# Kernel optimization log

Hardware: AMD Instinct MI355X
Metric: run time of the kernel (lower is better)

Reference implementation:

```python
import jax, jax.numpy as jnp
import numpy as np

N_NODES = 50000
N_EDGES = 800000
D_IN = 128
D_OUT = 128
BN_EPS = 1e-5


def setup_inputs() -> dict:
    key = jax.random.key(0)
    ks = jax.random.split(key, 8)
    node_feats = jax.random.normal(ks[0], (N_NODES, D_IN), dtype=jnp.float32)
    src = jax.random.randint(ks[1], (N_EDGES,), 0, N_NODES, dtype=jnp.int32)
    dst = jax.random.randint(ks[2], (N_EDGES,), 0, N_NODES, dtype=jnp.int32)
    # Glorot-ish init for weights
    scale = 1.0 / np.sqrt(D_IN)
    W = jax.random.normal(ks[3], (D_IN, D_OUT), dtype=jnp.float32) * scale
    b = jnp.zeros((D_OUT,), dtype=jnp.float32)
    Wr = jax.random.normal(ks[4], (D_IN, D_OUT), dtype=jnp.float32) * scale
    br = jnp.zeros((D_OUT,), dtype=jnp.float32)
    gamma = jnp.ones((D_OUT,), dtype=jnp.float32)
    beta = jnp.zeros((D_OUT,), dtype=jnp.float32)
    return {"node_feats": node_feats, "src": src, "dst": dst, "W": W, "b": b,
            "Wr": Wr, "br": br, "gamma": gamma, "beta": beta}


def reference(node_feats, src, dst, W, b, Wr, br, gamma, beta):
    N = node_feats.shape[0]
    ones_e = jnp.ones(src.shape[0], dtype=node_feats.dtype)
    # DGL GraphConv norm='both': D_out^{-1/2} on source side, D_in^{-1/2} on dest side
    deg_out = jnp.clip(jax.ops.segment_sum(ones_e, src, num_segments=N), 1.0)
    deg_in = jnp.clip(jax.ops.segment_sum(ones_e, dst, num_segments=N), 1.0)
    h = node_feats * jax.lax.rsqrt(deg_out)[:, None]        # [N, D_in]
    agg = jax.ops.segment_sum(h[src], dst, num_segments=N)  # gather + scatter-add, [N, D_in]
    agg = agg * jax.lax.rsqrt(deg_in)[:, None]
    gcn = jax.nn.relu(agg @ W + b)                           # GraphConv activation=relu
    res = jax.nn.relu(node_feats @ Wr + br)                  # residual branch
    y = gcn + res
    # BatchNorm1d (training mode: biased batch stats)
    mean = jnp.mean(y, axis=0)
    var = jnp.mean(jnp.square(y - mean), axis=0)
    out = (y - mean) * jax.lax.rsqrt(var + BN_EPS) * gamma + beta
    return out
```

## Files before the change

kernel.cpp:

```cpp
#include <hip/hip_runtime.h>

#define N_NODES 50000
#define N_EDGES 800000
#define D 128
#define BN_EPS 1e-5f
#define AGG_BLOCKS 2048
#define SCAN_BLOCKS 196
#define CHUNKS 64
#define EPC (N_EDGES / CHUNKS)
#define HALF_BINS 25600
#define HALF_U32 12800

typedef short bf16x8 __attribute__((ext_vector_type(8)));
typedef float f32x4  __attribute__((ext_vector_type(4)));


__global__ __launch_bounds__(256) void hist_kernel(
        const int* __restrict__ keys, unsigned int* __restrict__ hist) {
    __shared__ unsigned int h[HALF_U32];
    int tid = threadIdx.x;
    int c = blockIdx.x, r = blockIdx.y;
    for (int j = tid; j < HALF_U32; j += 256) h[j] = 0u;
    __syncthreads();
    int base = c * EPC;
    int lo = r * HALF_BINS;
    for (int i = tid; i < EPC; i += 256) {
        int b = keys[base + i] - lo;
        if ((unsigned)b < (unsigned)HALF_BINS)
            atomicAdd(&h[b >> 1], 1u << ((b & 1) * 16));
    }
    __syncthreads();
    unsigned int* out = hist + ((size_t)(r * CHUNKS + c)) * HALF_U32;
    for (int j = tid; j < HALF_U32; j += 256) out[j] = h[j];
}

__global__ __launch_bounds__(256) void merge_kernel(
        unsigned int* __restrict__ histD, unsigned int* __restrict__ histS,
        int* __restrict__ cnt_in, int* __restrict__ cnt_out) {
    int q = blockIdx.x * 256 + threadIdx.x;
    int r = blockIdx.y;
    unsigned int* hist = blockIdx.z ? histS : histD;
    int* cnt = blockIdx.z ? cnt_out : cnt_in;
    unsigned int lo = 0, hi = 0;
    for (int c = 0; c < CHUNKS; c++) {
        size_t idx = ((size_t)(r * CHUNKS + c)) * HALF_U32 + q;
        unsigned int v = hist[idx];
        hist[idx] = lo | (hi << 16);
        lo += v & 0xffffu; hi += v >> 16;
    }
    int n0 = r * HALF_BINS + q * 2;
    cnt[n0]     = (int)lo;
    cnt[n0 + 1] = (int)hi;
}

__global__ __launch_bounds__(256) void scan1_kernel(
        const int* __restrict__ cnt_in, int* __restrict__ row_ptr, int* __restrict__ blk_sum) {
    __shared__ int sh[256];
    int t = threadIdx.x;
    int i = blockIdx.x * 256 + t;
    int v = cnt_in[i];
    sh[t] = v;
    __syncthreads();
    int inc = v;
    #pragma unroll
    for (int off = 1; off < 256; off <<= 1) {
        int u = (t >= off) ? sh[t - off] : 0;
        __syncthreads();
        inc += u; sh[t] = inc;
        __syncthreads();
    }
    row_ptr[i] = inc - v;
    if (t == 255) blk_sum[blockIdx.x] = inc;
}

__global__ __launch_bounds__(256) void scan2_kernel(int* __restrict__ blk_sum, int* __restrict__ row_ptr) {
    __shared__ int sh[256];
    int t = threadIdx.x;
    int v = (t < SCAN_BLOCKS) ? blk_sum[t] : 0;
    sh[t] = v;
    __syncthreads();
    int inc = v;
    #pragma unroll
    for (int off = 1; off < 256; off <<= 1) {
        int u = (t >= off) ? sh[t - off] : 0;
        __syncthreads();
        inc += u; sh[t] = inc;
        __syncthreads();
    }
    if (t < SCAN_BLOCKS) blk_sum[t] = inc - v;
    if (t == 0) row_ptr[N_NODES] = N_EDGES;
}

__global__ __launch_bounds__(256) void scan3_kernel(
        const int* __restrict__ cnt_in, const int* __restrict__ cnt_out,
        const int* __restrict__ blk_sum, int* __restrict__ row_ptr,
        float* __restrict__ rin, float* __restrict__ rout) {
    int i = blockIdx.x * 256 + threadIdx.x;
    if (i < N_NODES) {
        row_ptr[i] = row_ptr[i] + blk_sum[blockIdx.x];
        int ci = cnt_in[i], co = cnt_out[i];
        rin[i]  = rsqrtf((float)(ci > 1 ? ci : 1));
        rout[i] = rsqrtf((float)(co > 1 ? co : 1));
    }
}

__global__ __launch_bounds__(512) void fill2_kernel(
        const int* __restrict__ src, const int* __restrict__ dst,
        const int* __restrict__ row_ptr, const unsigned int* __restrict__ histP,
        int* __restrict__ csr_src) {
    __shared__ unsigned int h[HALF_U32];
    int tid = threadIdx.x;
    int c = blockIdx.x;
    int base = c * EPC;
    for (int r = 0; r < 2; r++) {
        for (int j = tid; j < HALF_U32; j += 512) h[j] = 0u;
        __syncthreads();
        int lo = r * HALF_BINS;
        const unsigned int* pre_c = histP + ((size_t)(r * CHUNKS + c)) * HALF_U32;
        for (int i = tid; i < EPC; i += 512) {
            int d = dst[base + i];
            int b = d - lo;
            if ((unsigned)b < (unsigned)HALF_BINS) {
                int sh = (b & 1) * 16;
                unsigned int old = atomicAdd(&h[b >> 1], 1u << sh);
                unsigned int rank = (old >> sh) & 0xffffu;
                unsigned int pre = (pre_c[b >> 1] >> sh) & 0xffffu;
                int p = row_ptr[d] + (int)(pre + rank);
                csr_src[p] = src[base + i];
            }
        }
        __syncthreads();
    }
}

__device__ __forceinline__ unsigned int pack_rne(float a, float b) {
    unsigned int ua = __float_as_uint(a); ua += 0x7fffu + ((ua >> 16) & 1u);
    unsigned int ub = __float_as_uint(b); ub += 0x7fffu + ((ub >> 16) & 1u);
    return (ua >> 16) | (ub & 0xffff0000u);
}

__global__ __launch_bounds__(256) void pack_w(
        const float* __restrict__ W, const float* __restrict__ Wr,
        uint4* __restrict__ pW, uint4* __restrict__ pWr) {
    int t = blockIdx.x * 256 + threadIdx.x;
    const float* S = (t & 2048) ? Wr : W;
    uint4* Dst     = (t & 2048) ? pWr : pW;
    int e = t & 2047;
    int lane = e & 63, ks = (e >> 6) & 3, ct = e >> 8;
    int n  = ct * 16 + (lane & 15);
    int k0 = ks * 32 + (lane >> 4) * 8;
    float v[8];
    #pragma unroll
    for (int j = 0; j < 8; j++) v[j] = S[(k0 + j) * D + n];
    uint4 r;
    r.x = pack_rne(v[0], v[1]); r.y = pack_rne(v[2], v[3]);
    r.z = pack_rne(v[4], v[5]); r.w = pack_rne(v[6], v[7]);
    Dst[e] = r;
}

__global__ __launch_bounds__(256) void gemm_mfma(
        const float* __restrict__ x, const uint4* __restrict__ pW,
        const uint4* __restrict__ pWr, const float* __restrict__ br,
        const float* __restrict__ rout, unsigned short* __restrict__ hwb,
        float* __restrict__ res) {
    int tid = threadIdx.x, wid = tid >> 6, lane = tid & 63;
    int quad = lane >> 4, l15 = lane & 15;
    int r0 = blockIdx.x * 64 + wid * 16;
    int arow = r0 + l15; if (arow > N_NODES - 1) arow = N_NODES - 1;
    union { bf16x8 v; uint4 u; } A[4];
    const float* xrow = x + (size_t)arow * D;
    #pragma unroll
    for (int ks = 0; ks < 4; ks++) {
        float4 f0 = *(const float4*)(xrow + ks * 32 + quad * 8);
        float4 f1 = *(const float4*)(xrow + ks * 32 + quad * 8 + 4);
        A[ks].u.x = pack_rne(f0.x, f0.y); A[ks].u.y = pack_rne(f0.z, f0.w);
        A[ks].u.z = pack_rne(f1.x, f1.y); A[ks].u.w = pack_rne(f1.z, f1.w);
    }
    f32x4 accW[8], accR[8];
    #pragma unroll
    for (int ct = 0; ct < 8; ct++) { accW[ct] = (f32x4)0.f; accR[ct] = (f32x4)0.f; }
    #pragma unroll
    for (int ct = 0; ct < 8; ct++) {
        #pragma unroll
        for (int ks = 0; ks < 4; ks++) {
            union { bf16x8 v; uint4 u; } Bw, Br2;
            Bw.u  = pW [(ct * 4 + ks) * 64 + lane];
            Br2.u = pWr[(ct * 4 + ks) * 64 + lane];
            accW[ct] = __builtin_amdgcn_mfma_f32_16x16x32_bf16(A[ks].v, Bw.v,  accW[ct], 0, 0, 0);
            accR[ct] = __builtin_amdgcn_mfma_f32_16x16x32_bf16(A[ks].v, Br2.v, accR[ct], 0, 0, 0);
        }
    }
    float ro[4]; int rowok[4];
    #pragma unroll
    for (int reg = 0; reg < 4; reg++) {
        int row = r0 + quad * 4 + reg;
        rowok[reg] = row < N_NODES;
        ro[reg] = rout[rowok[reg] ? row : N_NODES - 1];
    }
    #pragma unroll
    for (int ct = 0; ct < 8; ct++) {
        int c = ct * 16 + l15;
        float brv = br[c];
        #pragma unroll
        for (int reg = 0; reg < 4; reg++) {
            int row = r0 + quad * 4 + reg;
            if (rowok[reg]) {
                float hv = accW[ct][reg] * ro[reg];
                unsigned int u = __float_as_uint(hv);
                u += 0x7fffu + ((u >> 16) & 1u);
                hwb[(size_t)row * D + c] = (unsigned short)(u >> 16);
                res[(size_t)row * D + c] = fmaxf(accR[ct][reg] + brv, 0.f);
            }
        }
    }
}

__device__ __forceinline__ float bf_lo(unsigned int v) { return __uint_as_float(v << 16); }
__device__ __forceinline__ float bf_hi(unsigned int v) { return __uint_as_float(v & 0xffff0000u); }

__device__ __forceinline__ void acc8(float* a, const uint4 v) {
    a[0] += bf_lo(v.x); a[1] += bf_hi(v.x);
    a[2] += bf_lo(v.y); a[3] += bf_hi(v.y);
    a[4] += bf_lo(v.z); a[5] += bf_hi(v.z);
    a[6] += bf_lo(v.w); a[7] += bf_hi(v.w);
}
__device__ __forceinline__ void acc8m(float* a, const uint4 v, float m) {
    a[0] = fmaf(m, bf_lo(v.x), a[0]); a[1] = fmaf(m, bf_hi(v.x), a[1]);
    a[2] = fmaf(m, bf_lo(v.y), a[2]); a[3] = fmaf(m, bf_hi(v.y), a[3]);
    a[4] = fmaf(m, bf_lo(v.z), a[4]); a[5] = fmaf(m, bf_hi(v.z), a[5]);
    a[6] = fmaf(m, bf_lo(v.w), a[6]); a[7] = fmaf(m, bf_hi(v.w), a[7]);
}

__device__ __forceinline__ int sel4(int qg, int i0, int i1, int i2, int i3) {
    int a = (qg & 1) ? i1 : i0;
    int b = (qg & 1) ? i3 : i2;
    return (qg & 2) ? b : a;
}

__global__ __launch_bounds__(256) void agg_kernel(
        const unsigned int* __restrict__ hwb, const int* __restrict__ row_ptr,
        const int* __restrict__ csr_src, const float* __restrict__ rin,
        const float* __restrict__ bias, float* __restrict__ y,
        float* __restrict__ parts) {
    __shared__ float red[4 * 256];
    int tid = threadIdx.x;
    int lane = tid & 63, wid = tid >> 6;
    int wave = blockIdx.x * 4 + wid;
    int nw = AGG_BLOCKS * 4;
    int qg = lane >> 4;
    int ql = lane & 15;
    float s1[8] = {0,0,0,0,0,0,0,0}, s2[8] = {0,0,0,0,0,0,0,0};
    float4 bv0, bv1;
    if (lane < 16) {
        bv0 = ((const float4*)bias)[2 * lane];
        bv1 = ((const float4*)bias)[2 * lane + 1];
    }
    for (int n = wave; n < N_NODES; n += nw) {
        int e0 = row_ptr[n], e1 = row_ptr[n + 1];
        float a[8] = {0,0,0,0,0,0,0,0};
        for (int j0 = e0; j0 < e1; j0 += 64) {
            int cnt = e1 - j0; if (cnt > 64) cnt = 64;
            int myidx = (lane < cnt) ? csr_src[j0 + lane] : 0;
            int i = 0;
            for (; i + 16 <= cnt; i += 16) {
                int p0 = sel4(qg, __builtin_amdgcn_readlane(myidx, i + 0),
                                  __builtin_amdgcn_readlane(myidx, i + 1),
                                  __builtin_amdgcn_readlane(myidx, i + 2),
                                  __builtin_amdgcn_readlane(myidx, i + 3));
                int p1 = sel4(qg, __builtin_amdgcn_readlane(myidx, i + 4),
                                  __builtin_amdgcn_readlane(myidx, i + 5),
                                  __builtin_amdgcn_readlane(myidx, i + 6),
                                  __builtin_amdgcn_readlane(myidx, i + 7));
                int p2 = sel4(qg, __builtin_amdgcn_readlane(myidx, i + 8),
                                  __builtin_amdgcn_readlane(myidx, i + 9),
                                  __builtin_amdgcn_readlane(myidx, i + 10),
                                  __builtin_amdgcn_readlane(myidx, i + 11));
                int p3 = sel4(qg, __builtin_amdgcn_readlane(myidx, i + 12),
                                  __builtin_amdgcn_readlane(myidx, i + 13),
                                  __builtin_amdgcn_readlane(myidx, i + 14),
                                  __builtin_amdgcn_readlane(myidx, i + 15));
                uint4 v0 = *((const uint4*)(hwb + (size_t)p0 * 64) + ql);
                uint4 v1 = *((const uint4*)(hwb + (size_t)p1 * 64) + ql);
                uint4 v2 = *((const uint4*)(hwb + (size_t)p2 * 64) + ql);
                uint4 v3 = *((const uint4*)(hwb + (size_t)p3 * 64) + ql);
                acc8(a, v0); acc8(a, v1); acc8(a, v2); acc8(a, v3);
            }
            for (; i + 4 <= cnt; i += 4) {
                int p0 = sel4(qg, __builtin_amdgcn_readlane(myidx, i + 0),
                                  __builtin_amdgcn_readlane(myidx, i + 1),
                                  __builtin_amdgcn_readlane(myidx, i + 2),
                                  __builtin_amdgcn_readlane(myidx, i + 3));
                uint4 v0 = *((const uint4*)(hwb + (size_t)p0 * 64) + ql);
                acc8(a, v0);
            }
            int t = cnt - i;
            if (t > 0) {
                int lim = cnt - 1;
                int j1 = i + 1 <= lim ? i + 1 : lim;
                int j2 = i + 2 <= lim ? i + 2 : lim;
                int p0 = sel4(qg, __builtin_amdgcn_readlane(myidx, i),
                                  __builtin_amdgcn_readlane(myidx, j1),
                                  __builtin_amdgcn_readlane(myidx, j2),
                                  __builtin_amdgcn_readlane(myidx, lim));
                uint4 v0 = *((const uint4*)(hwb + (size_t)p0 * 64) + ql);
                float m = (qg < t) ? 1.f : 0.f;
                acc8m(a, v0, m);
            }
        }
        #pragma unroll
        for (int k = 0; k < 8; k++) {
            a[k] += __shfl_xor(a[k], 16);
            a[k] += __shfl_xor(a[k], 32);
        }
        if (lane < 16) {
            float ri = rin[n];
            float4* yv = (float4*)(y + (size_t)n * D);
            float4 r0 = yv[2 * lane], r1 = yv[2 * lane + 1];
            float o[8];
            o[0] = fmaxf(a[0] * ri + bv0.x, 0.f) + r0.x;
            o[1] = fmaxf(a[1] * ri + bv0.y, 0.f) + r0.y;
            o[2] = fmaxf(a[2] * ri + bv0.z, 0.f) + r0.z;
            o[3] = fmaxf(a[3] * ri + bv0.w, 0.f) + r0.w;
            o[4] = fmaxf(a[4] * ri + bv1.x, 0.f) + r1.x;
            o[5] = fmaxf(a[5] * ri + bv1.y, 0.f) + r1.y;
            o[6] = fmaxf(a[6] * ri + bv1.z, 0.f) + r1.z;
            o[7] = fmaxf(a[7] * ri + bv1.w, 0.f) + r1.w;
            yv[2 * lane]     = make_float4(o[0], o[1], o[2], o[3]);
            yv[2 * lane + 1] = make_float4(o[4], o[5], o[6], o[7]);
            #pragma unroll
            for (int k = 0; k < 8; k++) { s1[k] += o[k]; s2[k] += o[k] * o[k]; }
        }
    }
    if (lane < 16) {
        int c0 = lane * 8;
        #pragma unroll
        for (int k = 0; k < 8; k++) {
            red[wid * 256 + c0 + k]       = s1[k];
            red[wid * 256 + 128 + c0 + k] = s2[k];
        }
    }
    __syncthreads();
    if (tid < 256) {
        float v = red[tid] + red[256 + tid] + red[512 + tid] + red[768 + tid];
        parts[(size_t)blockIdx.x * 256 + tid] = v;
    }
}

__global__ __launch_bounds__(256) void bn_fin2(
        const float* __restrict__ parts, const float* __restrict__ gamma,
        const float* __restrict__ beta, float* __restrict__ scsh) {
    __shared__ float rs1[256], rs2[256];
    int c = blockIdx.x, t = threadIdx.x;
    float s1 = 0.f, s2 = 0.f;
    for (int b = t; b < AGG_BLOCKS; b += 256) {
        s1 += parts[(size_t)b * 256 + c];
        s2 += parts[(size_t)b * 256 + 128 + c];
    }
    rs1[t] = s1; rs2[t] = s2;
    __syncthreads();
    for (int off = 128; off > 0; off >>= 1) {
        if (t < off) { rs1[t] += rs1[t + off]; rs2[t] += rs2[t + off]; }
        __syncthreads();
    }
    if (t == 0) {
        const float invN = 1.0f / (float)N_NODES;
        float mean = rs1[0] * invN;
        float var  = rs2[0] * invN - mean * mean;
        float sc = gamma[c] * rsqrtf(var + BN_EPS);
        scsh[c] = sc;
        scsh[128 + c] = beta[c] - mean * sc;
    }
}

__global__ void norm_kernel(float* __restrict__ y, const float* __restrict__ scsh) {
    int i = blockIdx.x * blockDim.x + threadIdx.x;
    if (i < N_NODES * 32) {
        float4 v = ((float4*)y)[i];
        int c = (i & 31) * 4;
        v.x = v.x * scsh[c]     + scsh[128 + c];
        v.y = v.y * scsh[c + 1] + scsh[128 + c + 1];
        v.z = v.z * scsh[c + 2] + scsh[128 + c + 2];
        v.w = v.w * scsh[c + 3] + scsh[128 + c + 3];
        ((float4*)y)[i] = v;
    }
}

extern "C" void kernel_launch(void* const* d_in, const int* in_sizes, int n_in,
                              void* d_out, int out_size, void* d_ws, size_t ws_size,
                              hipStream_t stream) {
    const float* x     = (const float*)d_in[0];
    const int*   src   = (const int*)d_in[1];
    const int*   dst   = (const int*)d_in[2];
    const float* W     = (const float*)d_in[3];
    const float* b     = (const float*)d_in[4];
    const float* Wr    = (const float*)d_in[5];
    const float* br    = (const float*)d_in[6];
    const float* gamma = (const float*)d_in[7];
    const float* beta  = (const float*)d_in[8];
    float* out = (float*)d_out;

    char* ws = (char*)d_ws;
    int*   cnt_in  = (int*)(ws + 0);
    int*   cnt_out = (int*)(ws + 262144);
    int*   row_ptr = (int*)(ws + 524288);
    float* rin     = (float*)(ws + 1048576);
    float* rout    = (float*)(ws + 1310720);
    float* scsh    = (float*)(ws + 1576960);
    int*   blk_sum = (int*)(ws + 1579008);
    int*   csr_src = (int*)(ws + 1581056);
    unsigned short* hwb = (unsigned short*)(ws + 4800000);
    float* parts   = (float*)(ws + 17600000);
    uint4* pW      = (uint4*)(ws + 19697152);
    uint4* pWr     = (uint4*)(ws + 19729920);
    unsigned int* histD = (unsigned int*)(ws + 19762688);
    unsigned int* histS = (unsigned int*)(ws + 26316288);

    hist_kernel<<<dim3(CHUNKS, 2), 256, 0, stream>>>(dst, histD);
    hist_kernel<<<dim3(CHUNKS, 2), 256, 0, stream>>>(src, histS);
    merge_kernel<<<dim3(HALF_U32 / 256, 2, 2), 256, 0, stream>>>(histD, histS, cnt_in, cnt_out);
    scan1_kernel<<<SCAN_BLOCKS, 256, 0, stream>>>(cnt_in, row_ptr, blk_sum);
    scan2_kernel<<<1, 256, 0, stream>>>(blk_sum, row_ptr);
    scan3_kernel<<<SCAN_BLOCKS, 256, 0, stream>>>(cnt_in, cnt_out, blk_sum, row_ptr, rin, rout);
    fill2_kernel<<<CHUNKS, 512, 0, stream>>>(src, dst, row_ptr, histD, csr_src);
    pack_w<<<16, 256, 0, stream>>>(W, Wr, pW, pWr);
    gemm_mfma<<<(N_NODES + 63) / 64, 256, 0, stream>>>(x, pW, pWr, br, rout, hwb, out);
    agg_kernel<<<AGG_BLOCKS, 256, 0, stream>>>((const unsigned int*)hwb, row_ptr, csr_src, rin, b, out, parts);
    bn_fin2<<<128, 256, 0, stream>>>(parts, gamma, beta, scsh);
    norm_kernel<<<(N_NODES * 32 + 255) / 256, 256, 0, stream>>>(out, scsh);
}
```

Baseline: 254.4 us.

## Store residual branch in bf16, stage x via LDS, merge histogram launches

The GEMM now writes the residual ReLU output as bf16 into a reused workspace region (the histD area, which is no longer needed after the CSR fill), instead of fp32 into the output buffer. The aggregation kernel reads it with nontemporal loads, which halves residual write and read traffic. The GEMM also stages x into shared memory with coalesced float4 loads before building MFMA fragments, and the two histogram launches are merged into a single 3D grid. Storing the residual in bf16 adds rounding error before batch norm.

```diff
diff --git a/kernel.cpp b/kernel.cpp
--- a/kernel.cpp
+++ b/kernel.cpp
@@ -13,13 +13,17 @@
 
 typedef short bf16x8 __attribute__((ext_vector_type(8)));
 typedef float f32x4  __attribute__((ext_vector_type(4)));
+typedef unsigned int u32x4 __attribute__((ext_vector_type(4)));
 
 
 __global__ __launch_bounds__(256) void hist_kernel(
-        const int* __restrict__ keys, unsigned int* __restrict__ hist) {
+        const int* __restrict__ dst, const int* __restrict__ src,
+        unsigned int* __restrict__ histD, unsigned int* __restrict__ histS) {
     __shared__ unsigned int h[HALF_U32];
     int tid = threadIdx.x;
     int c = blockIdx.x, r = blockIdx.y;
+    const int* keys = blockIdx.z ? src : dst;
+    unsigned int* hist = blockIdx.z ? histS : histD;
     for (int j = tid; j < HALF_U32; j += 256) h[j] = 0u;
     __syncthreads();
     int base = c * EPC;
@@ -138,6 +142,10 @@
     unsigned int ub = __float_as_uint(b); ub += 0x7fffu + ((ub >> 16) & 1u);
     return (ua >> 16) | (ub & 0xffff0000u);
 }
+__device__ __forceinline__ unsigned short pack1_rne(float a) {
+    unsigned int ua = __float_as_uint(a); ua += 0x7fffu + ((ua >> 16) & 1u);
+    return (unsigned short)(ua >> 16);
+}
 
 __global__ __launch_bounds__(256) void pack_w(
         const float* __restrict__ W, const float* __restrict__ Wr,
@@ -162,20 +170,27 @@
         const float* __restrict__ x, const uint4* __restrict__ pW,
         const uint4* __restrict__ pWr, const float* __restrict__ br,
         const float* __restrict__ rout, unsigned short* __restrict__ hwb,
-        float* __restrict__ res) {
+        unsigned short* __restrict__ resb) {
+    __shared__ unsigned short xs[64][136];
     int tid = threadIdx.x, wid = tid >> 6, lane = tid & 63;
     int quad = lane >> 4, l15 = lane & 15;
-    int r0 = blockIdx.x * 64 + wid * 16;
-    int arow = r0 + l15; if (arow > N_NODES - 1) arow = N_NODES - 1;
-    union { bf16x8 v; uint4 u; } A[4];
-    const float* xrow = x + (size_t)arow * D;
-    #pragma unroll
-    for (int ks = 0; ks < 4; ks++) {
-        float4 f0 = *(const float4*)(xrow + ks * 32 + quad * 8);
-        float4 f1 = *(const float4*)(xrow + ks * 32 + quad * 8 + 4);
-        A[ks].u.x = pack_rne(f0.x, f0.y); A[ks].u.y = pack_rne(f0.z, f0.w);
-        A[ks].u.z = pack_rne(f1.x, f1.y); A[ks].u.w = pack_rne(f1.z, f1.w);
-    }
+    int r0b = blockIdx.x * 64;
+    const float4* xg = (const float4*)(x + (size_t)r0b * D);
+    int maxidx = (N_NODES - r0b) * (D / 4);
+    #pragma unroll
+    for (int i = 0; i < 8; i++) {
+        int idx = tid + 256 * i;
+        float4 v = (idx < maxidx) ? xg[idx] : make_float4(0.f, 0.f, 0.f, 0.f);
+        int row = idx >> 5, c0 = (idx & 31) * 4;
+        *(unsigned int*)&xs[row][c0]     = pack_rne(v.x, v.y);
+        *(unsigned int*)&xs[row][c0 + 2] = pack_rne(v.z, v.w);
+    }
+    __syncthreads();
+    int wrow0 = wid * 16;
+    bf16x8 A[4];
+    #pragma unroll
+    for (int ks = 0; ks < 4; ks++)
+        A[ks] = *(const bf16x8*)&xs[wrow0 + l15][ks * 32 + quad * 8];
     f32x4 accW[8], accR[8];
     #pragma unroll
     for (int ct = 0; ct < 8; ct++) { accW[ct] = (f32x4)0.f; accR[ct] = (f32x4)0.f; }
@@ -186,10 +201,11 @@
             union { bf16x8 v; uint4 u; } Bw, Br2;
             Bw.u  = pW [(ct * 4 + ks) * 64 + lane];
             Br2.u = pWr[(ct * 4 + ks) * 64 + lane];
-            accW[ct] = __builtin_amdgcn_mfma_f32_16x16x32_bf16(A[ks].v, Bw.v,  accW[ct], 0, 0, 0);
-            accR[ct] = __builtin_amdgcn_mfma_f32_16x16x32_bf16(A[ks].v, Br2.v, accR[ct], 0, 0, 0);
-        }
-    }
+            accW[ct] = __builtin_amdgcn_mfma_f32_16x16x32_bf16(A[ks], Bw.v,  accW[ct], 0, 0, 0);
+            accR[ct] = __builtin_amdgcn_mfma_f32_16x16x32_bf16(A[ks], Br2.v, accR[ct], 0, 0, 0);
+        }
+    }
+    int r0 = r0b + wrow0;
     float ro[4]; int rowok[4];
     #pragma unroll
     for (int reg = 0; reg < 4; reg++) {
@@ -205,11 +221,8 @@
         for (int reg = 0; reg < 4; reg++) {
             int row = r0 + quad * 4 + reg;
             if (rowok[reg]) {
-                float hv = accW[ct][reg] * ro[reg];
-                unsigned int u = __float_as_uint(hv);
-                u += 0x7fffu + ((u >> 16) & 1u);
-                hwb[(size_t)row * D + c] = (unsigned short)(u >> 16);
-                res[(size_t)row * D + c] = fmaxf(accR[ct][reg] + brv, 0.f);
+                hwb [(size_t)row * D + c] = pack1_rne(accW[ct][reg] * ro[reg]);
+                resb[(size_t)row * D + c] = pack1_rne(fmaxf(accR[ct][reg] + brv, 0.f));
             }
         }
     }
@@ -240,8 +253,8 @@
 __global__ __launch_bounds__(256) void agg_kernel(
         const unsigned int* __restrict__ hwb, const int* __restrict__ row_ptr,
         const int* __restrict__ csr_src, const float* __restrict__ rin,
-        const float* __restrict__ bias, float* __restrict__ y,
-        float* __restrict__ parts) {
+        const float* __restrict__ bias, const unsigned short* __restrict__ resb,
+        float* __restrict__ y, float* __restrict__ parts) {
     __shared__ float red[4 * 256];
     int tid = threadIdx.x;
     int lane = tid & 63, wid = tid >> 6;
@@ -257,10 +270,13 @@
     }
     for (int n = wave; n < N_NODES; n += nw) {
         int e0 = row_ptr[n], e1 = row_ptr[n + 1];
+        u32x4 rv4 = (u32x4)0u;
+        if (lane < 16)
+            rv4 = __builtin_nontemporal_load((const u32x4*)(resb + (size_t)n * D) + lane);
         float a[8] = {0,0,0,0,0,0,0,0};
         for (int j0 = e0; j0 < e1; j0 += 64) {
             int cnt = e1 - j0; if (cnt > 64) cnt = 64;
-            int myidx = (lane < cnt) ? csr_src[j0 + lane] : 0;
+            int myidx = (lane < cnt) ? __builtin_nontemporal_load(csr_src + j0 + lane) : 0;
             int i = 0;
             for (; i + 16 <= cnt; i += 16) {
                 int p0 = sel4(qg, __builtin_amdgcn_readlane(myidx, i + 0),
@@ -314,17 +330,16 @@
         }
         if (lane < 16) {
             float ri = rin[n];
+            float o[8];
+            o[0] = fmaxf(a[0] * ri + bv0.x, 0.f) + bf_lo(rv4.x);
+            o[1] = fmaxf(a[1] * ri + bv0.y, 0.f) + bf_hi(rv4.x);
+            o[2] = fmaxf(a[2] * ri + bv0.z, 0.f) + bf_lo(rv4.y);
+            o[3] = fmaxf(a[3] * ri + bv0.w, 0.f) + bf_hi(rv4.y);
+            o[4] = fmaxf(a[4] * ri + bv1.x, 0.f) + bf_lo(rv4.z);
+            o[5] = fmaxf(a[5] * ri + bv1.y, 0.f) + bf_hi(rv4.z);
+            o[6] = fmaxf(a[6] * ri + bv1.z, 0.f) + bf_lo(rv4.w);
+            o[7] = fmaxf(a[7] * ri + bv1.w, 0.f) + bf_hi(rv4.w);
             float4* yv = (float4*)(y + (size_t)n * D);
-            float4 r0 = yv[2 * lane], r1 = yv[2 * lane + 1];
-            float o[8];
-            o[0] = fmaxf(a[0] * ri + bv0.x, 0.f) + r0.x;
-            o[1] = fmaxf(a[1] * ri + bv0.y, 0.f) + r0.y;
-            o[2] = fmaxf(a[2] * ri + bv0.z, 0.f) + r0.z;
-            o[3] = fmaxf(a[3] * ri + bv0.w, 0.f) + r0.w;
-            o[4] = fmaxf(a[4] * ri + bv1.x, 0.f) + r1.x;
-            o[5] = fmaxf(a[5] * ri + bv1.y, 0.f) + r1.y;
-            o[6] = fmaxf(a[6] * ri + bv1.z, 0.f) + r1.z;
-            o[7] = fmaxf(a[7] * ri + bv1.w, 0.f) + r1.w;
             yv[2 * lane]     = make_float4(o[0], o[1], o[2], o[3]);
             yv[2 * lane + 1] = make_float4(o[4], o[5], o[6], o[7]);
             #pragma unroll
@@ -414,17 +429,17 @@
     uint4* pWr     = (uint4*)(ws + 19729920);
     unsigned int* histD = (unsigned int*)(ws + 19762688);
     unsigned int* histS = (unsigned int*)(ws + 26316288);
-
-    hist_kernel<<<dim3(CHUNKS, 2), 256, 0, stream>>>(dst, histD);
-    hist_kernel<<<dim3(CHUNKS, 2), 256, 0, stream>>>(src, histS);
+    unsigned short* resb = (unsigned short*)(ws + 19762688);
+
+    hist_kernel<<<dim3(CHUNKS, 2, 2), 256, 0, stream>>>(dst, src, histD, histS);
     merge_kernel<<<dim3(HALF_U32 / 256, 2, 2), 256, 0, stream>>>(histD, histS, cnt_in, cnt_out);
     scan1_kernel<<<SCAN_BLOCKS, 256, 0, stream>>>(cnt_in, row_ptr, blk_sum);
     scan2_kernel<<<1, 256, 0, stream>>>(blk_sum, row_ptr);
     scan3_kernel<<<SCAN_BLOCKS, 256, 0, stream>>>(cnt_in, cnt_out, blk_sum, row_ptr, rin, rout);
     fill2_kernel<<<CHUNKS, 512, 0, stream>>>(src, dst, row_ptr, histD, csr_src);
     pack_w<<<16, 256, 0, stream>>>(W, Wr, pW, pWr);
-    gemm_mfma<<<(N_NODES + 63) / 64, 256, 0, stream>>>(x, pW, pWr, br, rout, hwb, out);
-    agg_kernel<<<AGG_BLOCKS, 256, 0, stream>>>((const unsigned int*)hwb, row_ptr, csr_src, rin, b, out, parts);
+    gemm_mfma<<<(N_NODES + 63) / 64, 256, 0, stream>>>(x, pW, pWr, br, rout, hwb, resb);
+    agg_kernel<<<AGG_BLOCKS, 256, 0, stream>>>((const unsigned int*)hwb, row_ptr, csr_src, rin, b, resb, out, parts);
     bn_fin2<<<128, 256, 0, stream>>>(parts, gamma, beta, scsh);
     norm_kernel<<<(N_NODES * 32 + 255) / 256, 256, 0, stream>>>(out, scsh);
 }
```

Result: faster. 246.4 us (-3.2%).
